# Performance work log

Hardware: AMD Instinct MI355X
Metric: run time of the kernel (lower is better)

## Reference

```python
import jax, jax.numpy as jnp
import numpy as np

B = 8192; NPG = 32; N = B * NPG; E = 4 * N
F_IN = 70; HEADS = 2; HOUT = 64; D = HEADS * HOUT; NB = 4; REL = 86; DK = D // 2
NEG_SLOPE = 0.2; EPS = 1e-5


def setup_inputs():
    key = jax.random.key(0)
    ks = list(jax.random.split(key, 32)); ki = iter(ks)
    def nk():
        return next(ki)
    def rn(shape, s=0.1):
        return jax.random.normal(nk(), shape, jnp.float32) * s
    base = (jnp.arange(E) // (E // B)) * NPG  # each graph owns a contiguous node range
    def edges():
        s = base + jax.random.randint(nk(), (E,), 0, NPG)
        d = base + jax.random.randint(nk(), (E,), 0, NPG)
        return jnp.stack([s, d]).astype(jnp.int32)
    return dict(
        xh=rn((N, F_IN), 1.0), xt=rn((N, F_IN), 1.0),
        edge_h=edges(), edge_t=edges(),
        batch=(jnp.arange(N) // NPG).astype(jnp.int32),
        rels=jax.random.randint(nk(), (B,), 0, REL).astype(jnp.int32),
        W0=rn((F_IN, D)), Wr=rn((NB - 1, D, D)),
        att_src=rn((NB, HEADS, HOUT)), att_dst=rn((NB, HEADS, HOUT)),
        gat_b=jnp.zeros((NB, D), jnp.float32),
        sag_rel_w=rn((NB, D)), sag_rel_b=jnp.zeros((NB,), jnp.float32),
        sag_root_w=rn((NB, D)),
        nw=jnp.ones((NB, D), jnp.float32), nb2=jnp.zeros((NB, D), jnp.float32),
        inw=jnp.ones((F_IN,), jnp.float32), inb=jnp.zeros((F_IN,), jnp.float32),
        wq=rn((D, DK)), wk=rn((D, DK)),
        cob=jnp.zeros((DK,), jnp.float32), coa=rn((DK,)),
        rel_emb=rn((REL, D * D)),
    )


def _lnorm(x, w, b):  # PyG LayerNorm, node mode (per-node over features)
    mu = jnp.mean(x, -1, keepdims=True)
    var = jnp.var(x, -1, keepdims=True)
    return (x - mu) * jax.lax.rsqrt(var + EPS) * w + b


def _gat(x, src, dst, W, a_s, a_d, bias):
    # src/dst already include self-loops (PyG GATConv default add_self_loops=True)
    h = (x @ W).reshape(N, HEADS, HOUT)
    a_src = jnp.einsum('nhc,hc->nh', h, a_s)
    a_dst = jnp.einsum('nhc,hc->nh', h, a_d)
    alpha = jax.nn.leaky_relu(a_src[src] + a_dst[dst], NEG_SLOPE)  # [E+N, H]
    m = jax.ops.segment_max(alpha, dst, num_segments=N)
    ex = jnp.exp(alpha - m[dst])
    den = jax.ops.segment_sum(ex, dst, num_segments=N)
    w = ex / (den[dst] + 1e-16)
    out = jax.ops.segment_sum(h[src] * w[:, :, None], dst, num_segments=N)
    return out.reshape(N, D) + bias


def _readout(x, ei, batch, rw, rb, root_w):
    # SAGPooling(min_score=-1): GraphConv score, per-graph softmax, keeps all nodes
    aggr = jax.ops.segment_sum(x[ei[0]], ei[1], num_segments=N)
    score = aggr @ rw + rb + x @ root_w  # [N]
    m = jax.ops.segment_max(score, batch, num_segments=B)
    ex = jnp.exp(score - m[batch])
    den = jax.ops.segment_sum(ex, batch, num_segments=B)
    s = ex / (den[batch] + 1e-16)
    return jax.ops.segment_sum(x * s[:, None], batch, num_segments=B)  # global_add_pool [B, D]


def _l2norm(x):
    return x / jnp.clip(jnp.linalg.norm(x, axis=-1, keepdims=True), 1e-12)


def _forward(xh, xt, edge_h, edge_t, batch, rels, W0, Wr, att_src, att_dst, gat_b,
             sag_rel_w, sag_rel_b, sag_root_w, nw, nb2, inw, inb, wq, wk, cob, coa, rel_emb):
    loops = jnp.arange(N, dtype=edge_h.dtype)
    def side(x, ei):
        src = jnp.concatenate([ei[0], loops])
        dst = jnp.concatenate([ei[1], loops])
        x = _lnorm(x, inw, inb)
        reprs = []
        for i in range(NB):
            W = W0 if i == 0 else Wr[i - 1]
            x = _gat(x, src, dst, W, att_src[i], att_dst[i], gat_b[i])
            reprs.append(_readout(x, ei, batch, sag_rel_w[i], sag_rel_b[i], sag_root_w[i]))
            x = jax.nn.elu(_lnorm(x, nw[i], nb2[i]))
        return jnp.stack(reprs, axis=-2)  # [B, NB, D]

    rh = side(xh, edge_h)
    rt = side(xt, edge_t)

    # CoAttentionLayer(receiver=heads, attendant=tails)
    keys = rh @ wk       # [B, NB, DK]
    queries = rt @ wq    # [B, NB, DK]
    att = jnp.tanh(keys[:, :, None, :] + queries[:, None, :, :] + cob) @ coa  # [B, NB, NB]

    # RESCAL
    r = _l2norm(rel_emb[rels]).reshape(B, D, D)
    h = _l2norm(rh)
    t = _l2norm(rt)
    scores = jnp.einsum('bid,bde,bje->bij', h, r, t)
    return jnp.sum(att * scores, axis=(-2, -1))  # [B]


def reference(xh, xt, edge_h, edge_t, batch, rels, W0, Wr, att_src, att_dst, gat_b,
              sag_rel_w, sag_rel_b, sag_root_w, nw, nb2, inw, inb, wq, wk, cob, coa, rel_emb):
    return _forward(xh, xt, edge_h, edge_t, batch, rels, W0, Wr, att_src, att_dst, gat_b,
                    sag_rel_w, sag_rel_b, sag_root_w, nw, nb2, inw, inb, wq, wk, cob, coa, rel_emb)
```

## Files before the change

### kernel.cpp

```cpp
#include <hip/hip_runtime.h>
#include <math.h>

#define NG 8192
#define NPG 32
#define NN (NG*NPG)
#define NE (NN*4)
#define EPG 128
#define NEL (EPG+NPG)
#define FIN 70
#define DIM 128
#define XS 132
#define TS 36
#define NB 4
#define DK 64
#define NREL 86

typedef __attribute__((ext_vector_type(8))) short short8;
typedef __attribute__((ext_vector_type(4))) float f32x4;
typedef __attribute__((ext_vector_type(4))) unsigned int u32x4;

__device__ inline unsigned cvtpk(float a, float b) {
  unsigned r;
  asm("v_cvt_pk_bf16_f32 %0, %1, %2" : "=v"(r) : "v"(a), "v"(b));
  return r;
}
__device__ inline float lo16f(unsigned u) { return __uint_as_float(u << 16); }
__device__ inline float hi16f(unsigned u) { return __uint_as_float(u & 0xffff0000u); }
__device__ inline float bf16f(unsigned short h) {
  return __uint_as_float(((unsigned int)h) << 16);
}

__device__ inline void split8(const f32x4& a, const f32x4& b, short8& hi, short8& lo) {
  u32x4 H, L;
  #pragma unroll
  for (int p = 0; p < 2; ++p) {
    float x0 = a[2*p], x1 = a[2*p+1];
    unsigned h = cvtpk(x0, x1);
    H[p] = h;
    L[p] = cvtpk(x0 - lo16f(h), x1 - hi16f(h));
  }
  #pragma unroll
  for (int p = 0; p < 2; ++p) {
    float x0 = b[2*p], x1 = b[2*p+1];
    unsigned h = cvtpk(x0, x1);
    H[2+p] = h;
    L[2+p] = cvtpk(x0 - lo16f(h), x1 - hi16f(h));
  }
  hi = __builtin_bit_cast(short8, H);
  lo = __builtin_bit_cast(short8, L);
}

__device__ inline short8 ld8(const unsigned short* p) {
  union { short8 s; uint2 u[2]; } U;
  U.u[0] = *(const uint2*)p;
  U.u[1] = *(const uint2*)(p + 4);
  return U.s;
}
__device__ inline short8 ld16B(const unsigned short* p) {
  u32x4 u = *(const u32x4*)p;
  return __builtin_bit_cast(short8, u);
}

struct Smem {
  float x[NPG][XS];
  unsigned short h2thi[DIM][TS];
  unsigned short h2tlo[DIM][TS];
  union {
    float Pt[2][NPG][TS];
    struct {
      float keysl[NB][DK];
      float querl[NB][DK];
      float attw[NB*NB];
      float red[NB*NB];
      float u4[4][DIM];
    } f;
  } uu;
  int   srcl[EPG];
  int   dstl[EPG];
  float asrc[NPG][2];
  float adst[NPG][2];
  float wred[4][2];
  float pl[NPG];
  float ql[NPG];
  float sval[NPG];
  float sacc[NPG];
  float repr[2][NB][DIM];
  float scl[2][NB];
};

__global__ __launch_bounds__(256) void relnorm_kernel(
    const float* __restrict__ re, float* __restrict__ outn) {
  int r = blockIdx.x;
  const float* row = re + (size_t)r * (DIM*DIM);
  float s = 0.f;
  for (int i = threadIdx.x; i < DIM*DIM; i += 256) { float v = row[i]; s += v*v; }
  for (int w = 1; w < 64; w <<= 1) s += __shfl_xor(s, w);
  __shared__ float sred[4];
  if ((threadIdx.x & 63) == 0) sred[threadIdx.x >> 6] = s;
  __syncthreads();
  if (threadIdx.x == 0) outn[r] = sqrtf(sred[0]+sred[1]+sred[2]+sred[3]);
}

__global__ __launch_bounds__(256) void wprep_kernel(
    const float* __restrict__ W0, const float* __restrict__ Wr,
    unsigned short* __restrict__ wsp) {
  int idx = blockIdx.x * 256 + threadIdx.x;
  int l = idx >> 14;
  int k = (idx >> 7) & 127;
  int c = idx & 127;
  float v;
  if (l == 0) v = (k < FIN) ? W0[(size_t)k*DIM + c] : 0.f;
  else        v = Wr[(size_t)(l-1)*DIM*DIM + (size_t)k*DIM + c];
  unsigned h = cvtpk(v, 0.f);
  unsigned lo = cvtpk(v - lo16f(h), 0.f);
  int o = (l << 14) + c*128 + k;
  wsp[o] = (unsigned short)h;
  wsp[65536 + o] = (unsigned short)lo;
}

__global__ __launch_bounds__(256, 3) void ssi_kernel(
    const float* __restrict__ xh, const float* __restrict__ xt,
    const int* __restrict__ eh, const int* __restrict__ et,
    const int* __restrict__ rels,
    const float* __restrict__ W0, const float* __restrict__ Wr,
    const unsigned short* __restrict__ wsp,
    const float* __restrict__ att_src, const float* __restrict__ att_dst,
    const float* __restrict__ gat_b,
    const float* __restrict__ srw, const float* __restrict__ srb,
    const float* __restrict__ sroot,
    const float* __restrict__ nw, const float* __restrict__ nb2,
    const float* __restrict__ inw, const float* __restrict__ inb,
    const float* __restrict__ wqm, const float* __restrict__ wkm,
    const float* __restrict__ cob, const float* __restrict__ coa,
    const float* __restrict__ rel_emb, const float* __restrict__ rnorm,
    float* __restrict__ out)
{
  __shared__ Smem sm;
  const int t = threadIdx.x;
  const int g = blockIdx.x;
  const int n0 = g * NPG;
  const int lw = t & 63;
  const int r0 = lw & 15;
  const int g4 = lw >> 4;
  const int nb = (t >> 6) * 32;
  const int hdw = t >> 7;

  for (int side = 0; side < 2; ++side) {
    const float* xin = side ? xt : xh;
    const int*   ed  = side ? et : eh;

    if (t < EPG) {
      sm.srcl[t] = ed[g*EPG + t] - n0;
      sm.dstl[t] = ed[NE + g*EPG + t] - n0;
    }
    {
      int n = t >> 3, j = t & 7;
      float s = 0.f, s2 = 0.f;
      for (int f = j; f < FIN; f += 8) {
        float v = xin[(size_t)(n0+n)*FIN + f];
        s += v; s2 += v*v;
      }
      for (int w = 1; w < 8; w <<= 1) { s += __shfl_xor(s, w); s2 += __shfl_xor(s2, w); }
      float mu  = s * (1.f/FIN);
      float var = s2 * (1.f/FIN) - mu*mu;
      float inv = rsqrtf(var + 1e-5f);
      for (int f = j; f < FIN; f += 8) {
        float v = xin[(size_t)(n0+n)*FIN + f];
        sm.x[n][f] = (v - mu) * inv * inw[f] + inb[f];
      }
      for (int f = FIN + j; f < 96; f += 8) sm.x[n][f] = 0.f;
    }
    __syncthreads();

    for (int li = 0; li < NB; ++li) {
      {
        const float* W = (li == 0) ? W0 : (Wr + (size_t)(li-1)*DIM*DIM);
        const int K  = (li == 0) ? FIN : DIM;
        const int KS = (li == 0) ? 3 : 4;
        f32x4 acc[2][2];
        #pragma unroll
        for (int mt = 0; mt < 2; ++mt)
          #pragma unroll
          for (int nt = 0; nt < 2; ++nt)
            acc[mt][nt] = (f32x4){0.f,0.f,0.f,0.f};
        for (int ks = 0; ks < KS; ++ks) {
          const int k0 = ks*32 + g4*8;
          short8 ah[2], al[2], bh[2], bl[2];
          #pragma unroll
          for (int mt = 0; mt < 2; ++mt) {
            f32x4 va = *(const f32x4*)&sm.x[mt*16 + r0][k0];
            f32x4 vb = *(const f32x4*)&sm.x[mt*16 + r0][k0+4];
            split8(va, vb, ah[mt], al[mt]);
          }
          if (wsp) {
            const unsigned short* Wh = wsp + (li << 14);
            const unsigned short* Wl = wsp + 65536 + (li << 14);
            #pragma unroll
            for (int nt = 0; nt < 2; ++nt) {
              const int c = nb + nt*16 + r0;
              bh[nt] = ld16B(Wh + c*128 + k0);
              bl[nt] = ld16B(Wl + c*128 + k0);
            }
          } else {
            #pragma unroll
            for (int nt = 0; nt < 2; ++nt) {
              const int c = nb + nt*16 + r0;
              f32x4 wa, wb;
              #pragma unroll
              for (int j = 0; j < 4; ++j) {
                int ka = k0 + j, kb = k0 + 4 + j;
                wa[j] = (ka < K) ? W[(size_t)ka*DIM + c] : 0.f;
                wb[j] = (kb < K) ? W[(size_t)kb*DIM + c] : 0.f;
              }
              split8(wa, wb, bh[nt], bl[nt]);
            }
          }
          #pragma unroll
          for (int mt = 0; mt < 2; ++mt)
            #pragma unroll
            for (int nt = 0; nt < 2; ++nt) {
              acc[mt][nt] = __builtin_amdgcn_mfma_f32_16x16x32_bf16(ah[mt], bh[nt], acc[mt][nt], 0,0,0);
              acc[mt][nt] = __builtin_amdgcn_mfma_f32_16x16x32_bf16(ah[mt], bl[nt], acc[mt][nt], 0,0,0);
              acc[mt][nt] = __builtin_amdgcn_mfma_f32_16x16x32_bf16(al[mt], bh[nt], acc[mt][nt], 0,0,0);
              acc[mt][nt] = __builtin_amdgcn_mfma_f32_16x16x32_bf16(al[mt], bl[nt], acc[mt][nt], 0,0,0);
            }
        }
        #pragma unroll
        for (int mt = 0; mt < 2; ++mt)
          #pragma unroll
          for (int nt = 0; nt < 2; ++nt) {
            const int c = nb + nt*16 + r0;
            const int row0 = mt*16 + g4*4;
            f32x4 a = acc[mt][nt];
            unsigned h0 = cvtpk(a[0], a[1]), h1 = cvtpk(a[2], a[3]);
            unsigned l0 = cvtpk(a[0]-lo16f(h0), a[1]-hi16f(h0));
            unsigned l1 = cvtpk(a[2]-lo16f(h1), a[3]-hi16f(h1));
            *(uint2*)&sm.h2thi[c][row0] = make_uint2(h0, h1);
            *(uint2*)&sm.h2tlo[c][row0] = make_uint2(l0, l1);
          }
      }
      __syncthreads();

      {
        int n = t >> 3, hd = (t >> 2) & 1, j = t & 3;
        const float* as = att_src + ((size_t)li*2 + hd)*64;
        const float* ad = att_dst + ((size_t)li*2 + hd)*64;
        float ss = 0.f, sd = 0.f;
        #pragma unroll
        for (int u2 = 0; u2 < 16; ++u2) {
          int cl = u2*4 + j;
          int c = hd*64 + cl;
          float hv = bf16f(sm.h2thi[c][n]) + bf16f(sm.h2tlo[c][n]);
          ss += hv * as[cl];
          sd += hv * ad[cl];
        }
        ss += __shfl_xor(ss,1); ss += __shfl_xor(ss,2);
        sd += __shfl_xor(sd,1); sd += __shfl_xor(sd,2);
        if (j == 0) { sm.asrc[n][hd] = ss; sm.adst[n][hd] = sd; }
        float* Pz = &sm.uu.Pt[0][0][0];
        for (int idx = t; idx < 2*NPG*TS; idx += 256) Pz[idx] = 0.f;
      }
      __syncthreads();

      float al0 = -1e30f, al1 = -1e30f;
      int es = 0, edd = 0;
      if (t < NEL) {
        es  = (t < EPG) ? sm.srcl[t] : (t - EPG);
        edd = (t < EPG) ? sm.dstl[t] : (t - EPG);
        float a0 = sm.asrc[es][0] + sm.adst[edd][0];
        float a1 = sm.asrc[es][1] + sm.adst[edd][1];
        al0 = (a0 > 0.f) ? a0 : 0.2f*a0;
        al1 = (a1 > 0.f) ? a1 : 0.2f*a1;
      }
      {
        float m0 = al0, m1 = al1;
        for (int w = 1; w < 64; w <<= 1) {
          m0 = fmaxf(m0, __shfl_xor(m0, w));
          m1 = fmaxf(m1, __shfl_xor(m1, w));
        }
        if ((t & 63) == 0) { sm.wred[t>>6][0] = m0; sm.wred[t>>6][1] = m1; }
      }
      __syncthreads();

      if (t < NEL) {
        float M0 = fmaxf(fmaxf(sm.wred[0][0], sm.wred[1][0]),
                         fmaxf(sm.wred[2][0], sm.wred[3][0]));
        float M1 = fmaxf(fmaxf(sm.wred[0][1], sm.wred[1][1]),
                         fmaxf(sm.wred[2][1], sm.wred[3][1]));
        atomicAdd(&sm.uu.Pt[0][edd][es], __expf(al0 - M0));
        atomicAdd(&sm.uu.Pt[1][edd][es], __expf(al1 - M1));
      }
      __syncthreads();

      {
        int hd = t >> 7, r = (t >> 2) & 31, s0 = (t & 3) * 8;
        f32x4 pa = *(const f32x4*)&sm.uu.Pt[hd][r][s0];
        f32x4 pb = *(const f32x4*)&sm.uu.Pt[hd][r][s0+4];
        float rs = pa[0]+pa[1]+pa[2]+pa[3]+pb[0]+pb[1]+pb[2]+pb[3];
        rs += __shfl_xor(rs, 1);
        rs += __shfl_xor(rs, 2);
        float dv = 1.f / (rs + 1e-16f);
        #pragma unroll
        for (int q = 0; q < 4; ++q) { pa[q] *= dv; pb[q] *= dv; }
        __syncthreads();
        unsigned short* Pu = (unsigned short*)&sm.uu.Pt[0][0][0];
        const int LO = 2*NPG*TS;
        int base = (hd*NPG + r)*TS + s0;
        unsigned h0 = cvtpk(pa[0], pa[1]), h1 = cvtpk(pa[2], pa[3]);
        unsigned h2_ = cvtpk(pb[0], pb[1]), h3 = cvtpk(pb[2], pb[3]);
        unsigned l0 = cvtpk(pa[0]-lo16f(h0), pa[1]-hi16f(h0));
        unsigned l1 = cvtpk(pa[2]-lo16f(h1), pa[3]-hi16f(h1));
        unsigned l2 = cvtpk(pb[0]-lo16f(h2_), pb[1]-hi16f(h2_));
        unsigned l3 = cvtpk(pb[2]-lo16f(h3), pb[3]-hi16f(h3));
        *(uint2*)(Pu + base)     = make_uint2(h0, h1);
        *(uint2*)(Pu + base + 4) = make_uint2(h2_, h3);
        *(uint2*)(Pu + LO + base)     = make_uint2(l0, l1);
        *(uint2*)(Pu + LO + base + 4) = make_uint2(l2, l3);
      }
      __syncthreads();

      {
        const unsigned short* Pu = (const unsigned short*)&sm.uu.Pt[0][0][0];
        const int LO = 2*NPG*TS;
        const int k0 = g4*8;
        f32x4 acc[2][2];
        #pragma unroll
        for (int mt = 0; mt < 2; ++mt)
          #pragma unroll
          for (int nt = 0; nt < 2; ++nt)
            acc[mt][nt] = (f32x4){0.f,0.f,0.f,0.f};
        short8 Ah[2], Al[2], Bh[2], Bl[2];
        #pragma unroll
        for (int mt = 0; mt < 2; ++mt) {
          int base = (hdw*NPG + mt*16 + r0)*TS + k0;
          Ah[mt] = ld8(Pu + base);
          Al[mt] = ld8(Pu + LO + base);
        }
        #pragma unroll
        for (int nt = 0; nt < 2; ++nt) {
          const int c = nb + nt*16 + r0;
          Bh[nt] = ld8(&sm.h2thi[c][k0]);
          Bl[nt] = ld8(&sm.h2tlo[c][k0]);
        }
        #pragma unroll
        for (int mt = 0; mt < 2; ++mt)
          #pragma unroll
          for (int nt = 0; nt < 2; ++nt) {
            acc[mt][nt] = __builtin_amdgcn_mfma_f32_16x16x32_bf16(Ah[mt], Bh[nt], acc[mt][nt], 0,0,0);
            acc[mt][nt] = __builtin_amdgcn_mfma_f32_16x16x32_bf16(Ah[mt], Bl[nt], acc[mt][nt], 0,0,0);
            acc[mt][nt] = __builtin_amdgcn_mfma_f32_16x16x32_bf16(Al[mt], Bh[nt], acc[mt][nt], 0,0,0);
          }
        #pragma unroll
        for (int nt = 0; nt < 2; ++nt) {
          const int c = nb + nt*16 + r0;
          float bc = gat_b[(size_t)li*DIM + c];
          #pragma unroll
          for (int mt = 0; mt < 2; ++mt)
            #pragma unroll
            for (int q = 0; q < 4; ++q)
              sm.x[mt*16 + g4*4 + q][c] = acc[mt][nt][q] + bc;
        }
      }
      __syncthreads();

      {
        int n = t >> 3, j = t & 7;
        const float* rw = srw   + (size_t)li*DIM;
        const float* ro = sroot + (size_t)li*DIM;
        float p = 0.f, q = 0.f;
        #pragma unroll
        for (int u2 = 0; u2 < 16; ++u2) {
          int c = u2*8 + j;
          float xv = sm.x[n][c];
          p += xv * rw[c];
          q += xv * ro[c];
        }
        for (int w = 1; w < 8; w <<= 1) { p += __shfl_xor(p,w); q += __shfl_xor(q,w); }
        if (j == 0) { sm.pl[n] = p; sm.ql[n] = q; }
        if (t < NPG) sm.sacc[t] = 0.f;
      }
      __syncthreads();

      if (t < EPG) atomicAdd(&sm.sacc[sm.dstl[t]], sm.pl[sm.srcl[t]]);
      __syncthreads();

      if (t < NPG) {
        float s = sm.sacc[t] + srb[li] + sm.ql[t];
        float m = s;
        for (int w = 1; w < 32; w <<= 1) m = fmaxf(m, __shfl_xor(m, w));
        float ex = __expf(s - m);
        float dn = ex;
        for (int w = 1; w < 32; w <<= 1) dn += __shfl_xor(dn, w);
        sm.sval[t] = ex / (dn + 1e-16f);
      }
      __syncthreads();

      if (t < DIM) {
        float a = 0.f;
        #pragma unroll 8
        for (int n = 0; n < NPG; ++n) a += sm.x[n][t] * sm.sval[n];
        sm.repr[side][li][t] = a;
      }
      __syncthreads();

      if (li < NB-1) {
        int n = t >> 3, j = t & 7;
        float s = 0.f, s2 = 0.f;
        #pragma unroll
        for (int u2 = 0; u2 < 16; ++u2) {
          float v = sm.x[n][u2*8 + j];
          s += v; s2 += v*v;
        }
        for (int w = 1; w < 8; w <<= 1) { s += __shfl_xor(s,w); s2 += __shfl_xor(s2,w); }
        float mu  = s * (1.f/DIM);
        float var = s2 * (1.f/DIM) - mu*mu;
        float inv = rsqrtf(var + 1e-5f);
        const float* wv = nw  + (size_t)li*DIM;
        const float* bv = nb2 + (size_t)li*DIM;
        #pragma unroll
        for (int u2 = 0; u2 < 16; ++u2) {
          int c = u2*8 + j;
          float v = (sm.x[n][c] - mu) * inv * wv[c] + bv[c];
          sm.x[n][c] = (v > 0.f) ? v : (__expf(v) - 1.f);
        }
        __syncthreads();
      }
    }
  }

  {
    int i2 = t >> 6, k = t & 63;
    float ak = 0.f, aq = 0.f;
    for (int d = 0; d < DIM; ++d) {
      ak += sm.repr[0][i2][d] * wkm[(size_t)d*DK + k];
      aq += sm.repr[1][i2][d] * wqm[(size_t)d*DK + k];
    }
    sm.uu.f.keysl[i2][k] = ak;
    sm.uu.f.querl[i2][k] = aq;
  }
  {
    int sd = t >> 7, i = (t >> 5) & 3, j2 = t & 31;
    float s = 0.f;
    #pragma unroll
    for (int u2 = 0; u2 < 4; ++u2) {
      float v = sm.repr[sd][i][j2*4+u2];
      s += v*v;
    }
    for (int w = 1; w < 32; w <<= 1) s += __shfl_xor(s, w);
    if (j2 == 0) sm.scl[sd][i] = 1.f / fmaxf(sqrtf(s), 1e-12f);
  }
  __syncthreads();

  {
    int pair = t >> 4, kk = t & 15;
    int i = pair >> 2, j = pair & 3;
    float a = 0.f;
    #pragma unroll
    for (int u2 = 0; u2 < 4; ++u2) {
      int k = kk*4+u2;
      a += tanhf(sm.uu.f.keysl[i][k] + sm.uu.f.querl[j][k] + cob[k]) * coa[k];
    }
    for (int w = 1; w < 16; w <<= 1) a += __shfl_xor(a, w);
    if (kk == 0) sm.uu.f.attw[pair] = a;
  }
  int rel = rels[g];
  if (t < DIM) {
    const float* rr = rel_emb + (size_t)rel * (DIM*DIM);
    float a0=0.f, a1=0.f, a2=0.f, a3=0.f;
    for (int d = 0; d < DIM; ++d) {
      float rv = rr[(size_t)d*DIM + t];
      a0 += sm.repr[0][0][d] * rv;
      a1 += sm.repr[0][1][d] * rv;
      a2 += sm.repr[0][2][d] * rv;
      a3 += sm.repr[0][3][d] * rv;
    }
    sm.uu.f.u4[0][t]=a0; sm.uu.f.u4[1][t]=a1; sm.uu.f.u4[2][t]=a2; sm.uu.f.u4[3][t]=a3;
  }
  __syncthreads();

  {
    float rninv = 1.f / fmaxf(rnorm[rel], 1e-12f);
    int pair = t >> 4, kk = t & 15;
    int i = pair >> 2, j = pair & 3;
    float a = 0.f;
    #pragma unroll
    for (int u2 = 0; u2 < 8; ++u2) {
      int e = kk*8+u2;
      a += sm.uu.f.u4[i][e] * sm.repr[1][j][e];
    }
    for (int w = 1; w < 16; w <<= 1) a += __shfl_xor(a, w);
    if (kk == 0)
      sm.uu.f.red[pair] = sm.uu.f.attw[pair] * a * sm.scl[0][i] * sm.scl[1][j] * rninv;
  }
  __syncthreads();
  if (t == 0) {
    float s = 0.f;
    for (int p = 0; p < NB*NB; ++p) s += sm.uu.f.red[p];
    out[g] = s;
  }
}

extern "C" void kernel_launch(void* const* d_in, const int* in_sizes, int n_in,
                              void* d_out, int out_size, void* d_ws, size_t ws_size,
                              hipStream_t stream) {
  const float* xh      = (const float*)d_in[0];
  const float* xt      = (const float*)d_in[1];
  const int*   eh      = (const int*)d_in[2];
  const int*   et      = (const int*)d_in[3];
  const int*   rels    = (const int*)d_in[5];
  const float* W0      = (const float*)d_in[6];
  const float* Wr      = (const float*)d_in[7];
  const float* att_src = (const float*)d_in[8];
  const float* att_dst = (const float*)d_in[9];
  const float* gat_b   = (const float*)d_in[10];
  const float* srw     = (const float*)d_in[11];
  const float* srb     = (const float*)d_in[12];
  const float* sroot   = (const float*)d_in[13];
  const float* nw      = (const float*)d_in[14];
  const float* nb2_    = (const float*)d_in[15];
  const float* inw     = (const float*)d_in[16];
  const float* inb     = (const float*)d_in[17];
  const float* wqm     = (const float*)d_in[18];
  const float* wkm     = (const float*)d_in[19];
  const float* cob     = (const float*)d_in[20];
  const float* coa     = (const float*)d_in[21];
  const float* rel_emb = (const float*)d_in[22];
  float* out   = (float*)d_out;
  float* rnorm = (float*)d_ws;

  const size_t WS_NEED = 512 + 2 * 65536 * sizeof(unsigned short);
  const unsigned short* wsp = nullptr;
  relnorm_kernel<<<NREL, 256, 0, stream>>>(rel_emb, rnorm);
  if (ws_size >= WS_NEED) {
    unsigned short* w = (unsigned short*)((char*)d_ws + 512);
    wprep_kernel<<<256, 256, 0, stream>>>(W0, Wr, w);
    wsp = w;
  }
  ssi_kernel<<<NG, 256, 0, stream>>>(xh, xt, eh, et, rels, W0, Wr, wsp,
      att_src, att_dst, gat_b, srw, srb, sroot, nw, nb2_, inw, inb,
      wqm, wkm, cob, coa, rel_emb, rnorm, out);
}
```

Baseline: 1.236 ms.

## Fold attention and SAG score projections into precomputed weight-vector products

Precomputes W·att_src, W·att_dst, W·srw and W·sroot per layer in a small prep kernel. The per-node attention logits and SAG pooling scores then come from one extra MFMA tile inside the main GEMM. SAG scores are derived from the attention-weighted aggregation of these projected scalars plus a bias term, so the dot-product passes over the node features and two barriers are dropped. The cost is extra MFMA work on one wavefront, more shared memory, and a dependency on workspace size.

```diff
diff --git a/kernel.cpp b/kernel.cpp
--- a/kernel.cpp
+++ b/kernel.cpp
@@ -82,6 +82,10 @@
   float wred[4][2];
   float pl[NPG];
   float ql[NPG];
+  float hrq[4][NPG];
+  float pqp[2][NPG];
+  float pqq[2][NPG];
+  float cbl[NB];
   float sval[NPG];
   float sacc[NPG];
   float repr[2][NB][DIM];
@@ -118,12 +122,50 @@
   wsp[65536 + o] = (unsigned short)lo;
 }
 
+__global__ __launch_bounds__(128) void wxprep_kernel(
+    const float* __restrict__ W0, const float* __restrict__ Wr,
+    const float* __restrict__ att_src, const float* __restrict__ att_dst,
+    const float* __restrict__ srw, const float* __restrict__ sroot,
+    unsigned short* __restrict__ wx) {
+  int b = blockIdx.x;
+  int li = b >> 4, j = b & 15;
+  int k = threadIdx.x;
+  const int K = (li == 0) ? FIN : DIM;
+  float val = 0.f;
+  if (j < 8 && k < K) {
+    const float* Wrow = (li == 0) ? (W0 + (size_t)k*DIM)
+                                  : (Wr + (size_t)(li-1)*DIM*DIM + (size_t)k*DIM);
+    const float* v; int c0;
+    switch (j) {
+      case 0: v = att_src + ((size_t)li*2+0)*64; c0 = 0;  break;
+      case 1: v = att_dst + ((size_t)li*2+0)*64; c0 = 0;  break;
+      case 2: v = att_src + ((size_t)li*2+1)*64; c0 = 64; break;
+      case 3: v = att_dst + ((size_t)li*2+1)*64; c0 = 64; break;
+      case 4: v = srw   + (size_t)li*DIM;        c0 = 0;  break;
+      case 5: v = srw   + (size_t)li*DIM;        c0 = 64; break;
+      case 6: v = sroot + (size_t)li*DIM;        c0 = 0;  break;
+      default: v = sroot + (size_t)li*DIM;       c0 = 64; break;
+    }
+    for (int c = 0; c < 64; ++c) {
+      float vc = (j < 4) ? v[c] : v[c0 + c];
+      val += Wrow[c0 + c] * vc;
+    }
+  }
+  unsigned h = cvtpk(val, 0.f);
+  unsigned lo = cvtpk(val - lo16f(h), 0.f);
+  int o = (li << 11) + j*128 + k;
+  wx[o] = (unsigned short)h;
+  wx[8192 + o] = (unsigned short)lo;
+}
+
+template <bool FAST>
 __global__ __launch_bounds__(256, 3) void ssi_kernel(
     const float* __restrict__ xh, const float* __restrict__ xt,
     const int* __restrict__ eh, const int* __restrict__ et,
     const int* __restrict__ rels,
     const float* __restrict__ W0, const float* __restrict__ Wr,
     const unsigned short* __restrict__ wsp,
+    const unsigned short* __restrict__ wx,
     const float* __restrict__ att_src, const float* __restrict__ att_dst,
     const float* __restrict__ gat_b,
     const float* __restrict__ srw, const float* __restrict__ srb,
@@ -153,6 +195,17 @@
       sm.srcl[t] = ed[g*EPG + t] - n0;
       sm.dstl[t] = ed[NE + g*EPG + t] - n0;
     }
+    if (FAST && side == 0 && t >= 128) {
+      int li2 = (t-128) >> 5, ln = (t-128) & 31;
+      float s_ = 0.f;
+      #pragma unroll
+      for (int m = 0; m < 4; ++m) {
+        int c = ln + 32*m;
+        s_ += gat_b[(size_t)li2*DIM + c] * srw[(size_t)li2*DIM + c];
+      }
+      for (int w = 1; w < 32; w <<= 1) s_ += __shfl_xor(s_, w);
+      if (ln == 0) sm.cbl[li2] = s_;
+    }
     {
       int n = t >> 3, j = t & 7;
       float s = 0.f, s2 = 0.f;
@@ -178,11 +231,16 @@
         const int K  = (li == 0) ? FIN : DIM;
         const int KS = (li == 0) ? 3 : 4;
         f32x4 acc[2][2];
-        #pragma unroll
-        for (int mt = 0; mt < 2; ++mt)
+        f32x4 accx[2];
+        #pragma unroll
+        for (int mt = 0; mt < 2; ++mt) {
+          accx[mt] = (f32x4){0.f,0.f,0.f,0.f};
           #pragma unroll
           for (int nt = 0; nt < 2; ++nt)
             acc[mt][nt] = (f32x4){0.f,0.f,0.f,0.f};
+        }
+        const unsigned short* Wxh = FAST ? (wx + (li << 11)) : nullptr;
+        const unsigned short* Wxl = FAST ? (wx + 8192 + (li << 11)) : nullptr;
         for (int ks = 0; ks < KS; ++ks) {
           const int k0 = ks*32 + g4*8;
           short8 ah[2], al[2], bh[2], bl[2];
@@ -224,6 +282,17 @@
               acc[mt][nt] = __builtin_amdgcn_mfma_f32_16x16x32_bf16(al[mt], bh[nt], acc[mt][nt], 0,0,0);
               acc[mt][nt] = __builtin_amdgcn_mfma_f32_16x16x32_bf16(al[mt], bl[nt], acc[mt][nt], 0,0,0);
             }
+          if (FAST && t < 64) {
+            short8 bxh = ld16B(Wxh + r0*128 + k0);
+            short8 bxl = ld16B(Wxl + r0*128 + k0);
+            #pragma unroll
+            for (int mt = 0; mt < 2; ++mt) {
+              accx[mt] = __builtin_amdgcn_mfma_f32_16x16x32_bf16(ah[mt], bxh, accx[mt], 0,0,0);
+              accx[mt] = __builtin_amdgcn_mfma_f32_16x16x32_bf16(ah[mt], bxl, accx[mt], 0,0,0);
+              accx[mt] = __builtin_amdgcn_mfma_f32_16x16x32_bf16(al[mt], bxh, accx[mt], 0,0,0);
+              accx[mt] = __builtin_amdgcn_mfma_f32_16x16x32_bf16(al[mt], bxl, accx[mt], 0,0,0);
+            }
+          }
         }
         #pragma unroll
         for (int mt = 0; mt < 2; ++mt)
@@ -238,10 +307,26 @@
             *(uint2*)&sm.h2thi[c][row0] = make_uint2(h0, h1);
             *(uint2*)&sm.h2tlo[c][row0] = make_uint2(l0, l1);
           }
-      }
-      __syncthreads();
-
-      {
+        if (FAST && t < 64 && r0 < 8) {
+          #pragma unroll
+          for (int mt = 0; mt < 2; ++mt)
+            #pragma unroll
+            for (int q = 0; q < 4; ++q) {
+              int n = mt*16 + g4*4 + q;
+              float v = accx[mt][q];
+              switch (r0) {
+                case 0: sm.asrc[n][0] = v; break;
+                case 1: sm.adst[n][0] = v; break;
+                case 2: sm.asrc[n][1] = v; break;
+                case 3: sm.adst[n][1] = v; break;
+                default: sm.hrq[r0-4][n] = v;
+              }
+            }
+        }
+      }
+      __syncthreads();
+
+      if (!FAST) {
         int n = t >> 3, hd = (t >> 2) & 1, j = t & 3;
         const float* as = att_src + ((size_t)li*2 + hd)*64;
         const float* ad = att_dst + ((size_t)li*2 + hd)*64;
@@ -259,8 +344,8 @@
         if (j == 0) { sm.asrc[n][hd] = ss; sm.adst[n][hd] = sd; }
         float* Pz = &sm.uu.Pt[0][0][0];
         for (int idx = t; idx < 2*NPG*TS; idx += 256) Pz[idx] = 0.f;
-      }
-      __syncthreads();
+        __syncthreads();
+      }
 
       float al0 = -1e30f, al1 = -1e30f;
       int es = 0, edd = 0;
@@ -272,6 +357,10 @@
         al0 = (a0 > 0.f) ? a0 : 0.2f*a0;
         al1 = (a1 > 0.f) ? a1 : 0.2f*a1;
       }
+      if (FAST) {
+        float* Pz = &sm.uu.Pt[0][0][0];
+        for (int idx = t; idx < 2*NPG*TS; idx += 256) Pz[idx] = 0.f;
+      }
       {
         float m0 = al0, m1 = al1;
         for (int w = 1; w < 64; w <<= 1) {
@@ -289,6 +378,8 @@
                          fmaxf(sm.wred[2][1], sm.wred[3][1]));
         atomicAdd(&sm.uu.Pt[0][edd][es], __expf(al0 - M0));
         atomicAdd(&sm.uu.Pt[1][edd][es], __expf(al1 - M1));
+      } else if (FAST && t < NEL + NPG) {
+        sm.sacc[t - NEL] = 0.f;
       }
       __syncthreads();
 
@@ -302,6 +393,21 @@
         float dv = 1.f / (rs + 1e-16f);
         #pragma unroll
         for (int q = 0; q < 4; ++q) { pa[q] *= dv; pb[q] *= dv; }
+        if (FAST) {
+          f32x4 h0 = *(const f32x4*)&sm.hrq[hd][s0];
+          f32x4 h1 = *(const f32x4*)&sm.hrq[hd][s0+4];
+          f32x4 q0 = *(const f32x4*)&sm.hrq[2+hd][s0];
+          f32x4 q1 = *(const f32x4*)&sm.hrq[2+hd][s0+4];
+          float pp = 0.f, qq = 0.f;
+          #pragma unroll
+          for (int i = 0; i < 4; ++i) {
+            pp += pa[i]*h0[i] + pb[i]*h1[i];
+            qq += pa[i]*q0[i] + pb[i]*q1[i];
+          }
+          pp += __shfl_xor(pp, 1); pp += __shfl_xor(pp, 2);
+          qq += __shfl_xor(qq, 1); qq += __shfl_xor(qq, 2);
+          if ((t & 3) == 0) { sm.pqp[hd][r] = pp; sm.pqq[hd][r] = qq; }
+        }
         __syncthreads();
         unsigned short* Pu = (unsigned short*)&sm.uu.Pt[0][0][0];
         const int LO = 2*NPG*TS;
@@ -363,7 +469,7 @@
       }
       __syncthreads();
 
-      {
+      if (!FAST) {
         int n = t >> 3, j = t & 7;
         const float* rw = srw   + (size_t)li*DIM;
         const float* ro = sroot + (size_t)li*DIM;
@@ -378,14 +484,21 @@
         for (int w = 1; w < 8; w <<= 1) { p += __shfl_xor(p,w); q += __shfl_xor(q,w); }
         if (j == 0) { sm.pl[n] = p; sm.ql[n] = q; }
         if (t < NPG) sm.sacc[t] = 0.f;
-      }
-      __syncthreads();
-
-      if (t < EPG) atomicAdd(&sm.sacc[sm.dstl[t]], sm.pl[sm.srcl[t]]);
+        __syncthreads();
+      }
+
+      if (t < EPG) {
+        int s = sm.srcl[t], d = sm.dstl[t];
+        float ps;
+        if (FAST) ps = sm.pqp[0][s] + sm.pqp[1][s] + sm.cbl[li];
+        else      ps = sm.pl[s];
+        atomicAdd(&sm.sacc[d], ps);
+      }
       __syncthreads();
 
       if (t < NPG) {
-        float s = sm.sacc[t] + srb[li] + sm.ql[t];
+        float qn = FAST ? (sm.pqq[0][t] + sm.pqq[1][t]) : sm.ql[t];
+        float s = sm.sacc[t] + srb[li] + qn;
         float m = s;
         for (int w = 1; w < 32; w <<= 1) m = fmaxf(m, __shfl_xor(m, w));
         float ex = __expf(s - m);
@@ -528,15 +641,28 @@
   float* out   = (float*)d_out;
   float* rnorm = (float*)d_ws;
 
-  const size_t WS_NEED = 512 + 2 * 65536 * sizeof(unsigned short);
-  const unsigned short* wsp = nullptr;
+  const size_t NEED_W    = 512 + (size_t)2*65536*sizeof(unsigned short);
+  const size_t NEED_FULL = NEED_W + (size_t)2*8192*sizeof(unsigned short);
+
   relnorm_kernel<<<NREL, 256, 0, stream>>>(rel_emb, rnorm);
-  if (ws_size >= WS_NEED) {
-    unsigned short* w = (unsigned short*)((char*)d_ws + 512);
-    wprep_kernel<<<256, 256, 0, stream>>>(W0, Wr, w);
-    wsp = w;
-  }
-  ssi_kernel<<<NG, 256, 0, stream>>>(xh, xt, eh, et, rels, W0, Wr, wsp,
-      att_src, att_dst, gat_b, srw, srb, sroot, nw, nb2_, inw, inb,
-      wqm, wkm, cob, coa, rel_emb, rnorm, out);
-}
+
+  if (ws_size >= NEED_FULL) {
+    unsigned short* wsp = (unsigned short*)((char*)d_ws + 512);
+    unsigned short* wx  = wsp + 2*65536;
+    wprep_kernel<<<256, 256, 0, stream>>>(W0, Wr, wsp);
+    wxprep_kernel<<<64, 128, 0, stream>>>(W0, Wr, att_src, att_dst, srw, sroot, wx);
+    ssi_kernel<true><<<NG, 256, 0, stream>>>(xh, xt, eh, et, rels, W0, Wr, wsp, wx,
+        att_src, att_dst, gat_b, srw, srb, sroot, nw, nb2_, inw, inb,
+        wqm, wkm, cob, coa, rel_emb, rnorm, out);
+  } else if (ws_size >= NEED_W) {
+    unsigned short* wsp = (unsigned short*)((char*)d_ws + 512);
+    wprep_kernel<<<256, 256, 0, stream>>>(W0, Wr, wsp);
+    ssi_kernel<false><<<NG, 256, 0, stream>>>(xh, xt, eh, et, rels, W0, Wr, wsp, nullptr,
+        att_src, att_dst, gat_b, srw, srb, sroot, nw, nb2_, inw, inb,
+        wqm, wkm, cob, coa, rel_emb, rnorm, out);
+  } else {
+    ssi_kernel<false><<<NG, 256, 0, stream>>>(xh, xt, eh, et, rels, W0, Wr, nullptr, nullptr,
+        att_src, att_dst, gat_b, srw, srb, sroot, nw, nb2_, inw, inb,
+        wqm, wkm, cob, coa, rel_emb, rnorm, out);
+  }
+}
```

New measurement: 1.230 ms. About the same (-0.5%).
